# Optimization experiments

Measured on AMD Instinct MI355X. Metric: run time of the kernel, lower is better.

## Reference

```python
import jax, jax.numpy as jnp
import numpy as np

HEADS = 8
DIM_HEAD = 64
SCALE = DIM_HEAD ** -0.5
LN_EPS = 1e-5

def setup_inputs() -> dict:
    key = jax.random.key(0)
    k0, k1, k2 = jax.random.split(key, 3)
    B, S, D = 4, 2048, 512
    inner = HEADS * DIM_HEAD
    return {
        "x": jax.random.normal(k0, (B, S, D), dtype=jnp.float32),
        "ln_gamma": jnp.ones((D,), dtype=jnp.float32),
        "ln_beta": jnp.zeros((D,), dtype=jnp.float32),
        "w_qkv": jax.random.normal(k1, (D, 3 * inner), dtype=jnp.float32) * (D ** -0.5),
        "w_out": jax.random.normal(k2, (inner, D), dtype=jnp.float32) * (inner ** -0.5),
        "b_out": jnp.zeros((D,), dtype=jnp.float32),
    }

def reference(x, ln_gamma, ln_beta, w_qkv, w_out, b_out):
    B, S, D = x.shape
    # LayerNorm
    mu = jnp.mean(x, axis=-1, keepdims=True)
    var = jnp.mean(jnp.square(x - mu), axis=-1, keepdims=True)
    xn = (x - mu) * jax.lax.rsqrt(var + LN_EPS) * ln_gamma + ln_beta
    # QKV projection (no bias)
    qkv = xn @ w_qkv  # [B, S, 3*inner]
    q, k, v = jnp.split(qkv, 3, axis=-1)
    def to_heads(t):
        return t.reshape(B, S, HEADS, DIM_HEAD).transpose(0, 2, 1, 3)  # [B,H,S,Dh]
    q, k, v = to_heads(q), to_heads(k), to_heads(v)
    # Naive attention with materialized score matrix
    dots = jnp.einsum("bhsd,bhtd->bhst", q, k) * SCALE
    attn = jax.nn.softmax(dots, axis=-1)
    out = jnp.einsum("bhst,bhtd->bhsd", attn, v)
    out = out.transpose(0, 2, 1, 3).reshape(B, S, HEADS * DIM_HEAD)
    return out @ w_out + b_out
```

## Files before the change

### kernel.cpp

```cpp
#include <hip/hip_runtime.h>
#include <hip/hip_bf16.h>
#include <stdint.h>

typedef __bf16 bf16;
typedef __bf16 bf16x8 __attribute__((ext_vector_type(8)));
typedef __bf16 bf16x4 __attribute__((ext_vector_type(4)));
typedef float  f32x4  __attribute__((ext_vector_type(4)));

#define MFMA16(A, B, C) __builtin_amdgcn_mfma_f32_16x16x32_bf16((A), (B), (C), 0, 0, 0)

static constexpr int Bsz = 4, Seq = 2048, Dm = 512, Hh = 8, Dh = 64;

__device__ __forceinline__ void g2l_16(void* lds, const void* gp) {
  __builtin_amdgcn_global_load_lds((__attribute__((address_space(1))) void*)gp,
                                   (__attribute__((address_space(3))) void*)lds, 16, 0, 0);
}

__device__ __forceinline__ float max3f(float a, float b, float c) {
  return fmaxf(fmaxf(a, b), c);
}

__global__ __launch_bounds__(256) void ln_cast_kernel(
    const float* __restrict__ x, const float* __restrict__ g,
    const float* __restrict__ be, bf16* __restrict__ xn) {
  const int row  = blockIdx.x * 4 + (threadIdx.x >> 6);
  const int lane = threadIdx.x & 63;
  const f32x4* xr = (const f32x4*)(x + (size_t)row * Dm);
  f32x4 v0 = xr[lane];
  f32x4 v1 = xr[lane + 64];
  float s = (v0.x + v0.y + v0.z + v0.w) + (v1.x + v1.y + v1.z + v1.w);
#pragma unroll
  for (int off = 32; off > 0; off >>= 1) s += __shfl_xor(s, off);
  const float mu = s * (1.0f / Dm);
  f32x4 d0 = v0 - mu, d1 = v1 - mu;
  float q = d0.x * d0.x + d0.y * d0.y + d0.z * d0.z + d0.w * d0.w
          + d1.x * d1.x + d1.y * d1.y + d1.z * d1.z + d1.w * d1.w;
#pragma unroll
  for (int off = 32; off > 0; off >>= 1) q += __shfl_xor(q, off);
  const float rs = rsqrtf(q * (1.0f / Dm) + 1e-5f);
  const f32x4* gr = (const f32x4*)g;
  const f32x4* br = (const f32x4*)be;
  f32x4 g0 = gr[lane], g1 = gr[lane + 64];
  f32x4 b0 = br[lane], b1 = br[lane + 64];
  f32x4 y0 = d0 * rs * g0 + b0;
  f32x4 y1 = d1 * rs * g1 + b1;
  bf16x4 o0 = { (bf16)y0.x, (bf16)y0.y, (bf16)y0.z, (bf16)y0.w };
  bf16x4 o1 = { (bf16)y1.x, (bf16)y1.y, (bf16)y1.z, (bf16)y1.w };
  bf16x4* orow = (bf16x4*)(xn + (size_t)row * Dm);
  orow[lane]      = o0;
  orow[lane + 64] = o1;
}

__global__ __launch_bounds__(256) void tcast_kernel(
    const float* __restrict__ src, bf16* __restrict__ dst, int R, int C,
    int qrows, float qscale) {
  __shared__ float t[32][33];
  const int c0 = blockIdx.x * 32, r0 = blockIdx.y * 32;
  const int tx = threadIdx.x & 31, ty = threadIdx.x >> 5;
#pragma unroll
  for (int i = 0; i < 32; i += 8)
    t[ty + i][tx] = src[(size_t)(r0 + ty + i) * C + c0 + tx];
  __syncthreads();
#pragma unroll
  for (int i = 0; i < 32; i += 8) {
    const int rr = c0 + ty + i;
    const float sc = rr < qrows ? qscale : 1.0f;
    dst[(size_t)rr * R + r0 + tx] = (bf16)(t[tx][ty + i] * sc);
  }
}

__global__ __launch_bounds__(256) void gemm_qkv_kernel(
    const bf16* __restrict__ A,
    const bf16* __restrict__ Bt,
    bf16* __restrict__ Qb, bf16* __restrict__ Kb, bf16* __restrict__ VT) {
  constexpr int K = 512;
  __shared__ __align__(16) bf16 As[2][128 * 32];
  __shared__ __align__(16) bf16 Bs[2][128 * 32];
  const int m0 = blockIdx.x * 128, n0 = blockIdx.y * 128;
  const int tid = threadIdx.x, lane = tid & 63, wave = tid >> 6;
  const int lr = lane & 15, lg = lane >> 4;
  const int wm = (wave >> 1) * 64, wn = (wave & 1) * 64;
  const int srow = wave * 16 + (lane >> 2);
  const int scol = (lane & 3) * 8;
  const bf16* ga = A  + (size_t)(m0 + srow) * K + scol;
  const bf16* gb = Bt + (size_t)(n0 + srow) * K + scol;
  bf16* lA = &As[0][0] + wave * 512;
  bf16* lB = &Bs[0][0] + wave * 512;
  f32x4 acc[4][4] = {};

  auto STAGE = [&](int buf, int k0) {
    g2l_16(lA + buf * 4096,        ga + k0);
    g2l_16(lA + buf * 4096 + 2048, ga + (size_t)64 * K + k0);
    g2l_16(lB + buf * 4096,        gb + k0);
    g2l_16(lB + buf * 4096 + 2048, gb + (size_t)64 * K + k0);
  };
  auto COMPUTE = [&](int buf) {
    const bf16* as = &As[buf][0];
    const bf16* bs = &Bs[buf][0];
    bf16x8 af[4], bfr[4];
#pragma unroll
    for (int i = 0; i < 4; ++i)
      af[i] = *(const bf16x8*)&as[(wm + i * 16 + lr) * 32 + lg * 8];
#pragma unroll
    for (int j = 0; j < 4; ++j)
      bfr[j] = *(const bf16x8*)&bs[(wn + j * 16 + lr) * 32 + lg * 8];
#pragma unroll
    for (int i = 0; i < 4; ++i)
#pragma unroll
      for (int j = 0; j < 4; ++j)
        acc[i][j] = MFMA16(af[i], bfr[j], acc[i][j]);
  };

  STAGE(0, 0);
  asm volatile("s_waitcnt vmcnt(0)" ::: "memory");
  __syncthreads();
  for (int it = 0; it < 8; ++it) {
    STAGE(1, it * 64 + 32);
    COMPUTE(0);
    asm volatile("s_waitcnt vmcnt(0)" ::: "memory");
    __syncthreads();
    if (it < 7) STAGE(0, it * 64 + 64);
    COMPUTE(1);
    asm volatile("s_waitcnt vmcnt(0)" ::: "memory");
    __syncthreads();
  }
#pragma unroll
  for (int j = 0; j < 4; ++j) {
    const int n = n0 + wn + j * 16 + lr;
    const int which = n >> 9, h = (n >> 6) & 7, dh = n & 63;
    if (which < 2) {
      bf16* dst = which == 0 ? Qb : Kb;
#pragma unroll
      for (int i = 0; i < 4; ++i)
#pragma unroll
        for (int r = 0; r < 4; ++r) {
          const int m = m0 + wm + i * 16 + lg * 4 + r;
          const int b = m >> 11, s2 = m & 2047;
          dst[((size_t)((b * Hh + h) * Seq + s2) << 6) | dh] = (bf16)acc[i][j][r];
        }
    } else {
#pragma unroll
      for (int i = 0; i < 4; ++i)
#pragma unroll
        for (int r = 0; r < 4; ++r) {
          const int m = m0 + wm + i * 16 + lg * 4 + r;
          const int b = m >> 11, s2 = m & 2047;
          VT[((size_t)((b * Hh + h) * Dh + dh)) * Seq + s2] = (bf16)acc[i][j][r];
        }
    }
  }
}

__global__ __launch_bounds__(256) void gemm_out_kernel(
    const bf16* __restrict__ A,
    const bf16* __restrict__ Bt,
    const float* __restrict__ bias, float* __restrict__ out) {
  constexpr int K = 512;
  __shared__ __align__(16) bf16 As[2][128 * 32];
  __shared__ __align__(16) bf16 Bs[2][128 * 32];
  const int m0 = blockIdx.x * 128, n0 = blockIdx.y * 128;
  const int tid = threadIdx.x, lane = tid & 63, wave = tid >> 6;
  const int lr = lane & 15, lg = lane >> 4;
  const int wm = (wave >> 1) * 64, wn = (wave & 1) * 64;
  const int srow = wave * 16 + (lane >> 2);
  const int scol = (lane & 3) * 8;
  const bf16* ga = A  + (size_t)(m0 + srow) * K + scol;
  const bf16* gb = Bt + (size_t)(n0 + srow) * K + scol;
  bf16* lA = &As[0][0] + wave * 512;
  bf16* lB = &Bs[0][0] + wave * 512;
  f32x4 acc[4][4] = {};

  auto STAGE = [&](int buf, int k0) {
    g2l_16(lA + buf * 4096,        ga + k0);
    g2l_16(lA + buf * 4096 + 2048, ga + (size_t)64 * K + k0);
    g2l_16(lB + buf * 4096,        gb + k0);
    g2l_16(lB + buf * 4096 + 2048, gb + (size_t)64 * K + k0);
  };
  auto COMPUTE = [&](int buf) {
    const bf16* as = &As[buf][0];
    const bf16* bs = &Bs[buf][0];
    bf16x8 af[4], bfr[4];
#pragma unroll
    for (int i = 0; i < 4; ++i)
      af[i] = *(const bf16x8*)&as[(wm + i * 16 + lr) * 32 + lg * 8];
#pragma unroll
    for (int j = 0; j < 4; ++j)
      bfr[j] = *(const bf16x8*)&bs[(wn + j * 16 + lr) * 32 + lg * 8];
#pragma unroll
    for (int i = 0; i < 4; ++i)
#pragma unroll
      for (int j = 0; j < 4; ++j)
        acc[i][j] = MFMA16(af[i], bfr[j], acc[i][j]);
  };

  STAGE(0, 0);
  asm volatile("s_waitcnt vmcnt(0)" ::: "memory");
  __syncthreads();
  for (int it = 0; it < 8; ++it) {
    STAGE(1, it * 64 + 32);
    COMPUTE(0);
    asm volatile("s_waitcnt vmcnt(0)" ::: "memory");
    __syncthreads();
    if (it < 7) STAGE(0, it * 64 + 64);
    COMPUTE(1);
    asm volatile("s_waitcnt vmcnt(0)" ::: "memory");
    __syncthreads();
  }
#pragma unroll
  for (int j = 0; j < 4; ++j) {
    const int n = n0 + wn + j * 16 + lr;
    const float bv = bias[n];
#pragma unroll
    for (int i = 0; i < 4; ++i)
#pragma unroll
      for (int r = 0; r < 4; ++r) {
        const int m = m0 + wm + i * 16 + lg * 4 + r;
        out[(size_t)m * 512 + n] = acc[i][j][r] + bv;
      }
  }
}

__global__ __launch_bounds__(512) void attn9_kernel(
    const bf16* __restrict__ Qb, const bf16* __restrict__ Kb,
    const bf16* __restrict__ VT, bf16* __restrict__ OPn, float2* __restrict__ ML) {
  const int o   = blockIdx.x + gridDim.x * blockIdx.y;
  const int nid = ((o & 7) << 7) + (o >> 3);
  const int qs = nid & 31, bh = nid >> 5;
  const int qc = qs >> 1, sp = qs & 1;
  const int tid = threadIdx.x, lane = tid & 63, wave = tid >> 6;
  const int lr = lane & 15, lg = lane >> 4;
  const int q0 = qc * 128 + wave * 16;
  const bf16* Qh = Qb + (size_t)bh * Seq * Dh;
  const bf16* Kh = Kb + (size_t)bh * Seq * Dh;
  const bf16* Vh = VT + (size_t)bh * Dh * Seq;

  __shared__ __align__(16) bf16 KV[2][8192];
  __shared__ __align__(16) bf16 Pl[8][16][72];

  const int xs   = lr & 7;
  const int col0 = (lg ^ xs) * 8;
  const bf16* kv = &KV[0][0];
  const int kb0 = lr * 64 + col0;
  const int kb1 = lr * 64 + (col0 ^ 32);
  bf16* pw = &Pl[wave][lr][lg * 4];
  const bf16* pr = &Pl[wave][lr][lg * 8];

  const int krow = tid >> 3;
  const int kc   = (((tid & 7) ^ (krow & 7)) * 8);
  const bf16* gK = Kh + (size_t)(sp * 1024 + krow) * 64 + kc;
  const bf16* gV = Vh + (size_t)krow * Seq + sp * 1024 + kc;
  bf16* ldsD = &KV[0][0] + tid * 8;

  auto STAGE = [&](int dstOff, int t) {
    g2l_16(ldsD + dstOff,        gK + (size_t)t * 4096);
    g2l_16(ldsD + dstOff + 4096, gV + t * 64);
  };

  bf16x8 qf0 = *(const bf16x8*)&Qh[(size_t)(q0 + lr) * 64 + lg * 8];
  bf16x8 qf1 = *(const bf16x8*)&Qh[(size_t)(q0 + lr) * 64 + 32 + lg * 8];

  f32x4 oa[4] = {};
  f32x4 ol = {};
  float m = -1e30f;
  bf16x8 ones;
#pragma unroll
  for (int i = 0; i < 8; ++i) ones[i] = (bf16)1.0f;

  auto TILE = [&](int buf) {
    const int kB = buf * 8192;
    f32x4 st[4] = {};
#pragma unroll
    for (int c = 0; c < 4; ++c) {
      bf16x8 kf0 = *(const bf16x8*)&kv[kb0 + kB + c * 1024];
      bf16x8 kf1 = *(const bf16x8*)&kv[kb1 + kB + c * 1024];
      st[c] = MFMA16(kf0, qf0, st[c]);
      st[c] = MFMA16(kf1, qf1, st[c]);
    }
    float m0 = max3f(st[0][0], st[0][1], st[0][2]);
    float m1 = max3f(st[0][3], st[1][0], st[1][1]);
    float m2 = max3f(st[1][2], st[1][3], st[2][0]);
    float m3 = max3f(st[2][1], st[2][2], st[2][3]);
    float m4 = max3f(st[3][0], st[3][1], st[3][2]);
    float mx = max3f(max3f(m0, m1, m2), m3, fmaxf(m4, st[3][3]));
    mx = fmaxf(mx, __shfl_xor(mx, 16));
    mx = fmaxf(mx, __shfl_xor(mx, 32));
    if (__any(mx > m + 3.0f)) {
      const float mn = fmaxf(m, mx);
      const float al = exp2f(m - mn);
      m = mn;
#pragma unroll
      for (int j = 0; j < 4; ++j) {
        const float aj = __shfl(al, lg * 4 + j);
        ol[j] *= aj;
#pragma unroll
        for (int n = 0; n < 4; ++n) oa[n][j] *= aj;
      }
    }
#pragma unroll
    for (int c = 0; c < 4; ++c) {
      bf16x4 pk;
#pragma unroll
      for (int j = 0; j < 4; ++j) pk[j] = (bf16)exp2f(st[c][j] - m);
      *(bf16x4*)&pw[c * 16] = pk;
    }
    bf16x8 pf0 = *(const bf16x8*)&pr[0];
    bf16x8 pf1 = *(const bf16x8*)&pr[32];
    ol = MFMA16(pf0, ones, ol);
    ol = MFMA16(pf1, ones, ol);
#pragma unroll
    for (int n = 0; n < 4; ++n) {
      bf16x8 vf0 = *(const bf16x8*)&kv[kb0 + kB + 4096 + n * 1024];
      bf16x8 vf1 = *(const bf16x8*)&kv[kb1 + kB + 4096 + n * 1024];
      oa[n] = MFMA16(pf0, vf0, oa[n]);
      oa[n] = MFMA16(pf1, vf1, oa[n]);
    }
  };

  STAGE(0, 0);
  asm volatile("s_waitcnt vmcnt(0)" ::: "memory");
  __syncthreads();

  for (int it = 0; it < 8; ++it) {
    STAGE(8192, 2 * it + 1);
    TILE(0);
    asm volatile("s_waitcnt vmcnt(0)" ::: "memory");
    __syncthreads();
    if (it < 7) STAGE(0, 2 * it + 2);
    TILE(1);
    asm volatile("s_waitcnt vmcnt(0)" ::: "memory");
    __syncthreads();
  }

#pragma unroll
  for (int j = 0; j < 4; ++j) {
    const float mj = __shfl(m, lg * 4 + j);
    const float lj = 1.0f / ol[j];
    const int s2 = q0 + lg * 4 + j;
    const size_t row = (size_t)bh * Seq + s2;
#pragma unroll
    for (int n = 0; n < 4; ++n)
      OPn[((size_t)sp << 22) + row * 64 + n * 16 + lr] = (bf16)(oa[n][j] * lj);
    if (lr == 0) ML[(sp << 16) + row] = make_float2(mj, ol[j]);
  }
}

__global__ __launch_bounds__(256) void attn_combine_kernel(
    const bf16* __restrict__ OPn, const float2* __restrict__ ML,
    bf16* __restrict__ A2) {
  const int r = blockIdx.x * 4 + (threadIdx.x >> 6);
  const int d = threadIdx.x & 63;
  const float2 ml0 = ML[r];
  const float2 ml1 = ML[65536 + r];
  const float M  = fmaxf(ml0.x, ml1.x);
  const float a0 = exp2f(ml0.x - M) * ml0.y;
  const float a1 = exp2f(ml1.x - M) * ml1.y;
  const float inv = 1.0f / (a0 + a1);
  const float v0 = (float)OPn[(size_t)r * 64 + d];
  const float v1 = (float)OPn[(size_t)(1 << 22) + (size_t)r * 64 + d];
  const int bh = r >> 11, s = r & 2047;
  const int b = bh >> 3, h = bh & 7;
  A2[(size_t)(b * Seq + s) * 512 + h * 64 + d] = (bf16)((a0 * v0 + a1 * v1) * inv);
}

extern "C" void kernel_launch(void* const* d_in, const int* in_sizes, int n_in,
                              void* d_out, int out_size, void* d_ws, size_t ws_size,
                              hipStream_t stream) {
  const float* x    = (const float*)d_in[0];
  const float* gam  = (const float*)d_in[1];
  const float* bet  = (const float*)d_in[2];
  const float* wqkv = (const float*)d_in[3];
  const float* wout = (const float*)d_in[4];
  const float* bout = (const float*)d_in[5];
  float* out = (float*)d_out;

  bf16* xn    = (bf16*)d_ws;
  bf16* wqkvT = xn    + (size_t)8192 * 512;
  bf16* woutT = wqkvT + (size_t)1536 * 512;
  bf16* Qb    = woutT + (size_t)512 * 512;
  bf16* Kb    = Qb    + (size_t)4 * 8 * 2048 * 64;
  bf16* VT    = Kb    + (size_t)4 * 8 * 2048 * 64;
  bf16* OPn   = VT    + (size_t)4 * 8 * 2048 * 64;
  float2* ML  = (float2*)(OPn + ((size_t)2 << 22));
  bf16* A2    = xn;

  const float K1 = 0.18033688011112042f;

  ln_cast_kernel<<<2048, 256, 0, stream>>>(x, gam, bet, xn);
  tcast_kernel<<<dim3(48, 16), 256, 0, stream>>>(wqkv, wqkvT, 512, 1536, 512, K1);
  tcast_kernel<<<dim3(16, 16), 256, 0, stream>>>(wout, woutT, 512, 512, 0, 1.0f);
  gemm_qkv_kernel<<<dim3(64, 12), 256, 0, stream>>>(xn, wqkvT, Qb, Kb, VT);
  attn9_kernel<<<dim3(32, 32), 512, 0, stream>>>(Qb, Kb, VT, OPn, ML);
  attn_combine_kernel<<<16384, 256, 0, stream>>>(OPn, ML, A2);
  gemm_out_kernel<<<dim3(64, 4), 256, 0, stream>>>(A2, woutT, bout, out);
}
```

Measured before the change: 120.3 us.

## Switch attention to 32x32x16 MFMA with register-resident P fragments

The attention kernel moves from 16x16x32 MFMA to 32x32x16 MFMA, so each wave handles 32 query rows and a block covers 256 queries, which halves the grid. The probability matrix is repacked into A-operand fragments in registers using cross-half shuffles, replacing the LDS round-trip. The row sum is now computed with scalar adds instead of an MFMA against a ones vector. Each K/V tile staged in LDS is reused across twice as many queries, at the cost of higher register pressure and fewer blocks to spread across CUs.

```diff
diff --git a/kernel.cpp b/kernel.cpp
--- a/kernel.cpp
+++ b/kernel.cpp
@@ -5,9 +5,13 @@
 typedef __bf16 bf16;
 typedef __bf16 bf16x8 __attribute__((ext_vector_type(8)));
 typedef __bf16 bf16x4 __attribute__((ext_vector_type(4)));
+typedef __bf16 bf16x2 __attribute__((ext_vector_type(2)));
 typedef float  f32x4  __attribute__((ext_vector_type(4)));
+typedef float  f32x16 __attribute__((ext_vector_type(16)));
+typedef int    i32x4  __attribute__((ext_vector_type(4)));
 
 #define MFMA16(A, B, C) __builtin_amdgcn_mfma_f32_16x16x32_bf16((A), (B), (C), 0, 0, 0)
+#define MFMA32(A, B, C) __builtin_amdgcn_mfma_f32_32x32x16_bf16((A), (B), (C), 0, 0, 0)
 
 static constexpr int Bsz = 4, Seq = 2048, Dm = 512, Hh = 8, Dh = 64;
 
@@ -18,6 +22,11 @@
 
 __device__ __forceinline__ float max3f(float a, float b, float c) {
   return fmaxf(fmaxf(a, b), c);
+}
+
+__device__ __forceinline__ int pk2(float x, float y) {
+  bf16x2 t; t[0] = (bf16)x; t[1] = (bf16)y;
+  return __builtin_bit_cast(int, t);
 }
 
 __global__ __launch_bounds__(256) void ln_cast_kernel(
@@ -220,30 +229,23 @@
   }
 }
 
-__global__ __launch_bounds__(512) void attn9_kernel(
+__global__ __launch_bounds__(512) void attn10_kernel(
     const bf16* __restrict__ Qb, const bf16* __restrict__ Kb,
     const bf16* __restrict__ VT, bf16* __restrict__ OPn, float2* __restrict__ ML) {
   const int o   = blockIdx.x + gridDim.x * blockIdx.y;
-  const int nid = ((o & 7) << 7) + (o >> 3);
-  const int qs = nid & 31, bh = nid >> 5;
+  const int nid = ((o & 7) << 6) + (o >> 3);
+  const int qs = nid & 15, bh = nid >> 4;
   const int qc = qs >> 1, sp = qs & 1;
   const int tid = threadIdx.x, lane = tid & 63, wave = tid >> 6;
-  const int lr = lane & 15, lg = lane >> 4;
-  const int q0 = qc * 128 + wave * 16;
+  const int q_l = lane & 31, h5 = lane >> 5;
+  const int kx  = q_l & 7;
+  const int q0w = qc * 256 + wave * 32;
   const bf16* Qh = Qb + (size_t)bh * Seq * Dh;
   const bf16* Kh = Kb + (size_t)bh * Seq * Dh;
   const bf16* Vh = VT + (size_t)bh * Dh * Seq;
 
   __shared__ __align__(16) bf16 KV[2][8192];
-  __shared__ __align__(16) bf16 Pl[8][16][72];
-
-  const int xs   = lr & 7;
-  const int col0 = (lg ^ xs) * 8;
   const bf16* kv = &KV[0][0];
-  const int kb0 = lr * 64 + col0;
-  const int kb1 = lr * 64 + (col0 ^ 32);
-  bf16* pw = &Pl[wave][lr][lg * 4];
-  const bf16* pr = &Pl[wave][lr][lg * 8];
 
   const int krow = tid >> 3;
   const int kc   = (((tid & 7) ^ (krow & 7)) * 8);
@@ -256,63 +258,83 @@
     g2l_16(ldsD + dstOff + 4096, gV + t * 64);
   };
 
-  bf16x8 qf0 = *(const bf16x8*)&Qh[(size_t)(q0 + lr) * 64 + lg * 8];
-  bf16x8 qf1 = *(const bf16x8*)&Qh[(size_t)(q0 + lr) * 64 + 32 + lg * 8];
-
-  f32x4 oa[4] = {};
-  f32x4 ol = {};
-  float m = -1e30f;
-  bf16x8 ones;
-#pragma unroll
-  for (int i = 0; i < 8; ++i) ones[i] = (bf16)1.0f;
+  bf16x8 qfr[4];
+#pragma unroll
+  for (int s = 0; s < 4; ++s)
+    qfr[s] = *(const bf16x8*)&Qh[(size_t)(q0w + q_l) * 64 + 16 * s + 8 * h5];
+
+  f32x16 oa0 = {}, oa1 = {};
+  float m = -1e30f, ls = 0.0f;
+
+  auto mkfrag = [&](float p0, float p1, float p2, float p3,
+                    float p4, float p5, float p6, float p7) -> bf16x8 {
+    const int A = pk2(p0, p1), B = pk2(p2, p3), C = pk2(p4, p5), D = pk2(p6, p7);
+    const int sxA = __shfl_xor(A, 32), sxB = __shfl_xor(B, 32);
+    const int sxC = __shfl_xor(C, 32), sxD = __shfl_xor(D, 32);
+    i32x4 w = { h5 ? sxC : A, h5 ? sxD : B, h5 ? C : sxA, h5 ? D : sxB };
+    return __builtin_bit_cast(bf16x8, w);
+  };
 
   auto TILE = [&](int buf) {
     const int kB = buf * 8192;
-    f32x4 st[4] = {};
-#pragma unroll
-    for (int c = 0; c < 4; ++c) {
-      bf16x8 kf0 = *(const bf16x8*)&kv[kb0 + kB + c * 1024];
-      bf16x8 kf1 = *(const bf16x8*)&kv[kb1 + kB + c * 1024];
-      st[c] = MFMA16(kf0, qf0, st[c]);
-      st[c] = MFMA16(kf1, qf1, st[c]);
-    }
-    float m0 = max3f(st[0][0], st[0][1], st[0][2]);
-    float m1 = max3f(st[0][3], st[1][0], st[1][1]);
-    float m2 = max3f(st[1][2], st[1][3], st[2][0]);
-    float m3 = max3f(st[2][1], st[2][2], st[2][3]);
-    float m4 = max3f(st[3][0], st[3][1], st[3][2]);
-    float mx = max3f(max3f(m0, m1, m2), m3, fmaxf(m4, st[3][3]));
-    mx = fmaxf(mx, __shfl_xor(mx, 16));
+    f32x16 st0 = {}, st1 = {};
+#pragma unroll
+    for (int s = 0; s < 4; ++s) {
+      const int eoff = ((2 * s + h5) ^ kx) << 3;
+      bf16x8 kf0 = *(const bf16x8*)&kv[kB + q_l * 64 + eoff];
+      bf16x8 kf1 = *(const bf16x8*)&kv[kB + (32 + q_l) * 64 + eoff];
+      st0 = MFMA32(kf0, qfr[s], st0);
+      st1 = MFMA32(kf1, qfr[s], st1);
+    }
+    float mx = max3f(st0[0], st0[1], st1[0]);
+#pragma unroll
+    for (int r = 1; r < 8; ++r) mx = max3f(st0[2 * r], st0[2 * r + 1], mx);
+#pragma unroll
+    for (int r = 0; r < 5; ++r) mx = max3f(st1[2 * r + 1], st1[2 * r + 2], mx);
+    mx = max3f(st1[11], st1[12], mx);
+    mx = max3f(st1[13], st1[14], mx);
+    mx = fmaxf(st1[15], mx);
     mx = fmaxf(mx, __shfl_xor(mx, 32));
     if (__any(mx > m + 3.0f)) {
       const float mn = fmaxf(m, mx);
       const float al = exp2f(m - mn);
       m = mn;
-#pragma unroll
-      for (int j = 0; j < 4; ++j) {
-        const float aj = __shfl(al, lg * 4 + j);
-        ol[j] *= aj;
-#pragma unroll
-        for (int n = 0; n < 4; ++n) oa[n][j] *= aj;
+      ls *= al;
+#pragma unroll
+      for (int r = 0; r < 16; ++r) {
+        const int qr = (r & 3) + 8 * (r >> 2) + 4 * h5;
+        const float aj = __shfl(al, qr);
+        oa0[r] *= aj; oa1[r] *= aj;
       }
     }
 #pragma unroll
-    for (int c = 0; c < 4; ++c) {
-      bf16x4 pk;
-#pragma unroll
-      for (int j = 0; j < 4; ++j) pk[j] = (bf16)exp2f(st[c][j] - m);
-      *(bf16x4*)&pw[c * 16] = pk;
-    }
-    bf16x8 pf0 = *(const bf16x8*)&pr[0];
-    bf16x8 pf1 = *(const bf16x8*)&pr[32];
-    ol = MFMA16(pf0, ones, ol);
-    ol = MFMA16(pf1, ones, ol);
-#pragma unroll
-    for (int n = 0; n < 4; ++n) {
-      bf16x8 vf0 = *(const bf16x8*)&kv[kb0 + kB + 4096 + n * 1024];
-      bf16x8 vf1 = *(const bf16x8*)&kv[kb1 + kB + 4096 + n * 1024];
-      oa[n] = MFMA16(pf0, vf0, oa[n]);
-      oa[n] = MFMA16(pf1, vf1, oa[n]);
+    for (int i = 0; i < 16; ++i) {
+      st0[i] = exp2f(st0[i] - m);
+      st1[i] = exp2f(st1[i] - m);
+    }
+    {
+      float t0 = 0, t1 = 0, t2 = 0, t3 = 0;
+#pragma unroll
+      for (int i = 0; i < 4; ++i) {
+        t0 += st0[i] + st0[i + 4];  t1 += st0[i + 8] + st0[i + 12];
+        t2 += st1[i] + st1[i + 4];  t3 += st1[i + 8] + st1[i + 12];
+      }
+      float ps = (t0 + t1) + (t2 + t3);
+      ps += __shfl_xor(ps, 32);
+      ls += ps;
+    }
+    bf16x8 pa0 = mkfrag(st0[0], st0[1], st0[2],  st0[3],  st0[4],  st0[5],  st0[6],  st0[7]);
+    bf16x8 pa1 = mkfrag(st0[8], st0[9], st0[10], st0[11], st0[12], st0[13], st0[14], st0[15]);
+    bf16x8 pa2 = mkfrag(st1[0], st1[1], st1[2],  st1[3],  st1[4],  st1[5],  st1[6],  st1[7]);
+    bf16x8 pa3 = mkfrag(st1[8], st1[9], st1[10], st1[11], st1[12], st1[13], st1[14], st1[15]);
+#pragma unroll
+    for (int s = 0; s < 4; ++s) {
+      const bf16x8 pa = s == 0 ? pa0 : s == 1 ? pa1 : s == 2 ? pa2 : pa3;
+      const int eoff = ((2 * s + h5) ^ kx) << 3;
+      bf16x8 vf0 = *(const bf16x8*)&kv[kB + 4096 + q_l * 64 + eoff];
+      bf16x8 vf1 = *(const bf16x8*)&kv[kB + 4096 + (32 + q_l) * 64 + eoff];
+      oa0 = MFMA32(pa, vf0, oa0);
+      oa1 = MFMA32(pa, vf1, oa1);
     }
   };
 
@@ -332,15 +354,17 @@
   }
 
 #pragma unroll
-  for (int j = 0; j < 4; ++j) {
-    const float mj = __shfl(m, lg * 4 + j);
-    const float lj = 1.0f / ol[j];
-    const int s2 = q0 + lg * 4 + j;
-    const size_t row = (size_t)bh * Seq + s2;
-#pragma unroll
-    for (int n = 0; n < 4; ++n)
-      OPn[((size_t)sp << 22) + row * 64 + n * 16 + lr] = (bf16)(oa[n][j] * lj);
-    if (lr == 0) ML[(sp << 16) + row] = make_float2(mj, ol[j]);
+  for (int r = 0; r < 16; ++r) {
+    const int qr = (r & 3) + 8 * (r >> 2) + 4 * h5;
+    const float lr_ = __shfl(ls, qr);
+    const float mj  = __shfl(m, qr);
+    const float inv = 1.0f / lr_;
+    const size_t row = (size_t)bh * Seq + q0w + qr;
+    OPn[((size_t)sp << 22) + row * 64 + q_l]      = (bf16)(oa0[r] * inv);
+    OPn[((size_t)sp << 22) + row * 64 + 32 + q_l] = (bf16)(oa1[r] * inv);
+    if (lane == 0 || q_l == 0) {
+      if (q_l == 0) ML[(sp << 16) + row] = make_float2(mj, lr_);
+    }
   }
 }
 
@@ -389,7 +413,7 @@
   tcast_kernel<<<dim3(48, 16), 256, 0, stream>>>(wqkv, wqkvT, 512, 1536, 512, K1);
   tcast_kernel<<<dim3(16, 16), 256, 0, stream>>>(wout, woutT, 512, 512, 0, 1.0f);
   gemm_qkv_kernel<<<dim3(64, 12), 256, 0, stream>>>(xn, wqkvT, Qb, Kb, VT);
-  attn9_kernel<<<dim3(32, 32), 512, 0, stream>>>(Qb, Kb, VT, OPn, ML);
+  attn10_kernel<<<dim3(16, 32), 512, 0, stream>>>(Qb, Kb, VT, OPn, ML);
   attn_combine_kernel<<<16384, 256, 0, stream>>>(OPn, ML, A2);
   gemm_out_kernel<<<dim3(64, 4), 256, 0, stream>>>(A2, woutT, bout, out);
 }
```

After: 129.5 us. 7.7% more time.
